# Optimization experiments

Measured on AMD Instinct MI355X. Metric: run time of the kernel, lower is better.

The kernel has to match this reference:

```python
import jax, jax.numpy as jnp
import numpy as np

D_MODEL = 128
VOCAB = 4096
N_LAYERS = 4
D_FF = 512
D_INNER = 2 * D_MODEL      # Mamba expand=2
D_STATE = 16               # Mamba default
D_CONV = 4                 # Mamba default
DT_RANK = 8                # ceil(d_model/16)
B, L = 8, 4096


def setup_inputs() -> dict:
    key = jax.random.key(0)
    ks = jax.random.split(key, 12)
    def n(k, shp, sc=0.02):
        return jax.random.normal(k, shp, dtype=jnp.float32) * sc
    A0 = jnp.tile(jnp.arange(1, D_STATE + 1, dtype=jnp.float32)[None, None, :], (N_LAYERS, D_INNER, 1))
    return {
        "tokens": jax.random.randint(ks[0], (B, L), 0, VOCAB),
        "emb": n(ks[1], (VOCAB, D_MODEL)),
        "ln_w": jnp.ones((N_LAYERS, D_MODEL), jnp.float32),
        "ln_b": jnp.zeros((N_LAYERS, D_MODEL), jnp.float32),
        "W_in": n(ks[2], (N_LAYERS, D_MODEL, 2 * D_INNER)),
        "conv_w": n(ks[3], (N_LAYERS, D_INNER, 1, D_CONV), 0.2),
        "conv_b": jnp.zeros((N_LAYERS, D_INNER), jnp.float32),
        "W_xproj": n(ks[4], (N_LAYERS, D_INNER, DT_RANK + 2 * D_STATE)),
        "W_dt": n(ks[5], (N_LAYERS, DT_RANK, D_INNER), 0.1),
        "b_dt": jnp.full((N_LAYERS, D_INNER), -4.6, jnp.float32),  # softplus ~ 0.01
        "A_log": jnp.log(A0),
        "D_skip": jnp.ones((N_LAYERS, D_INNER), jnp.float32),
        "W_out": n(ks[6], (N_LAYERS, D_INNER, D_MODEL)),
        "W1": n(ks[7], (D_MODEL, D_FF)),
        "b1": jnp.zeros((D_FF,), jnp.float32),
        "W2": n(ks[8], (D_FF, VOCAB)),
        "b2": jnp.zeros((VOCAB,), jnp.float32),
    }


def _layer_norm(x, w, b):
    mu = x.mean(-1, keepdims=True)
    var = ((x - mu) ** 2).mean(-1, keepdims=True)
    return (x - mu) * jax.lax.rsqrt(var + 1e-5) * w + b


def _mamba(x, W_in, conv_w, conv_b, W_xproj, W_dt, b_dt, A_log, D_skip, W_out):
    # x: [B, L, d_model]
    xz = jnp.einsum('bld,de->ble', x, W_in)          # [B, L, 2*d_inner]
    xc, z = jnp.split(xz, 2, axis=-1)
    # depthwise causal conv over time
    xt = xc.swapaxes(1, 2)                            # [B, d_inner, L]
    xt = jax.lax.conv_general_dilated(
        xt, conv_w, window_strides=(1,), padding=[(D_CONV - 1, 0)],
        feature_group_count=D_INNER,
        dimension_numbers=('NCH', 'OIH', 'NCH')) + conv_b[None, :, None]
    u = jax.nn.silu(xt).swapaxes(1, 2)                # [B, L, d_inner]
    dbc = jnp.einsum('bld,de->ble', u, W_xproj)
    dt_r = dbc[..., :DT_RANK]
    Bm = dbc[..., DT_RANK:DT_RANK + D_STATE]          # [B, L, d_state]
    Cm = dbc[..., DT_RANK + D_STATE:]                 # [B, L, d_state]
    dt = jax.nn.softplus(jnp.einsum('blr,rd->bld', dt_r, W_dt) + b_dt)
    A = -jnp.exp(A_log)                               # [d_inner, d_state]

    def step(h, t):
        dt_t, B_t, C_t, u_t = t                       # [B,di], [B,ds], [B,ds], [B,di]
        dA = jnp.exp(dt_t[..., None] * A)             # [B, di, ds]
        h = dA * h + (dt_t * u_t)[..., None] * B_t[:, None, :]
        y = jnp.einsum('bds,bs->bd', h, C_t)
        return h, y

    xs = (dt.swapaxes(0, 1), Bm.swapaxes(0, 1), Cm.swapaxes(0, 1), u.swapaxes(0, 1))
    h0 = jnp.zeros((x.shape[0], D_INNER, D_STATE), x.dtype)
    _, ys = jax.lax.scan(step, h0, xs)                # [L, B, d_inner]
    y = ys.swapaxes(0, 1) + u * D_skip
    y = y * jax.nn.silu(z)
    return jnp.einsum('bld,de->ble', y, W_out)


def reference(tokens, emb, ln_w, ln_b, W_in, conv_w, conv_b, W_xproj, W_dt,
              b_dt, A_log, D_skip, W_out, W1, b1, W2, b2):
    x = emb[tokens]                                   # [B, L, d_model]
    for i in range(N_LAYERS):
        # source discards the residual returned by Block: x = mixer(norm(x))
        x = _mamba(_layer_norm(x, ln_w[i], ln_b[i]), W_in[i], conv_w[i],
                   conv_b[i], W_xproj[i], W_dt[i], b_dt[i], A_log[i],
                   D_skip[i], W_out[i])
    h = jax.nn.relu(jnp.einsum('bld,df->blf', x, W1) + b1)
    return jnp.einsum('blf,fv->blv', h, W2) + b2
```

## Files before the change

### kernel.cpp

```cpp
#include <hip/hip_runtime.h>
#include <hip/hip_bf16.h>

typedef __hip_bfloat16 bf16;
typedef __attribute__((ext_vector_type(8))) short short8;
typedef __attribute__((ext_vector_type(4))) float floatx4;

#define D_MODEL 128
#define VOCAB   4096
#define N_LAYERS 4
#define D_FF    512
#define D_INNER 256
#define D_STATE 16
#define DT_RANK 8
#define BATCH   8
#define SEQ     4096
#define NTOK    (BATCH*SEQ)
#define NCHUNK  16
#define CHUNK   256

__device__ __forceinline__ float bf2f(bf16 v) { return __bfloat162float(v); }
__device__ __forceinline__ bf16  f2bf(float v) { return __float2bfloat16(v); }

__device__ __forceinline__ void load_lds16(const void* g, void* l) {
  __builtin_amdgcn_global_load_lds(
      (const __attribute__((address_space(1))) unsigned int*)g,
      (__attribute__((address_space(3))) unsigned int*)l, 16, 0, 0);
}

__device__ __forceinline__ void store_out(float* p, float v) { *p = v; }
__device__ __forceinline__ void store_out(bf16* p, float v) { *p = f2bf(v); }

#define WT_TOTAL 2686976
__global__ void convw_kernel(const float* __restrict__ W_in,
                             const float* __restrict__ W_xproj,
                             const float* __restrict__ W_out,
                             const float* __restrict__ W1,
                             const float* __restrict__ W2,
                             bf16* __restrict__ Wt) {
  for (int o = blockIdx.x * blockDim.x + threadIdx.x; o < WT_TOTAL;
       o += gridDim.x * blockDim.x) {
    float v;
    if (o < 262144) {
      int l = o >> 16, r = o & 65535, n = r >> 7, k = r & 127;
      v = W_in[l * 65536 + k * 512 + n];
    } else if (o < 393216) {
      int p = o - 262144, l = p >> 15, r = p & 32767, n = r >> 8, k = r & 255;
      v = (n < 40) ? W_xproj[l * 10240 + k * 40 + n] : 0.f;
    } else if (o < 524288) {
      int p = o - 393216, l = p >> 15, r = p & 32767, n = r >> 8, k = r & 255;
      v = W_out[l * 32768 + k * 128 + n];
    } else if (o < 589824) {
      int p = o - 524288, n = p >> 7, k = p & 127;
      v = W1[k * 512 + n];
    } else {
      int p = o - 589824, n = p >> 9, k = p & 511;
      v = W2[k * 4096 + n];
    }
    Wt[o] = f2bf(v);
  }
}

__global__ void embed_kernel(const int* __restrict__ tokens,
                             const float* __restrict__ emb,
                             float* __restrict__ X) {
  int idx = blockIdx.x * 256 + threadIdx.x;
  int bl = idx >> 5, c = idx & 31;
  int tok = tokens[bl];
  ((float4*)X)[(long)bl * 32 + c] = ((const float4*)emb)[(long)tok * 32 + c];
}

__global__ __launch_bounds__(256) void ln_kernel(const float* __restrict__ X,
                                                 const float* __restrict__ w,
                                                 const float* __restrict__ b,
                                                 bf16* __restrict__ XN) {
  int wv = threadIdx.x >> 6, lane = threadIdx.x & 63;
  long row = (long)blockIdx.x * 4 + wv;
  const float* xp = X + row * 128;
  float2 v = *(const float2*)(xp + lane * 2);
  float s = v.x + v.y, q = v.x * v.x + v.y * v.y;
  #pragma unroll
  for (int o = 32; o; o >>= 1) {
    s += __shfl_xor(s, o, 64);
    q += __shfl_xor(q, o, 64);
  }
  float mu = s * (1.f / 128.f);
  float var = q * (1.f / 128.f) - mu * mu;
  float rs = rsqrtf(var + 1e-5f);
  int c = lane * 2;
  float o0 = (v.x - mu) * rs * w[c] + b[c];
  float o1 = (v.y - mu) * rs * w[c + 1] + b[c + 1];
  bf16* op = XN + row * 128 + c;
  op[0] = f2bf(o0);
  op[1] = f2bf(o1);
}

template <typename OutT>
__global__ __launch_bounds__(256) void gemm_kernel(
    const bf16* __restrict__ A, const bf16* __restrict__ Bt,
    OutT* __restrict__ C, const float* __restrict__ bias,
    int K, int N, int relu) {
  __shared__ __align__(16) bf16 As[128 * 64];
  __shared__ __align__(16) bf16 Bs[128 * 64];
  const int tid = threadIdx.x;
  const int lane = tid & 63;
  const int wave = tid >> 6;
  const int m0 = blockIdx.x * 128;
  const int n0 = blockIdx.y * 128;
  const int wm = (wave >> 1) * 64;
  const int wn = (wave & 1) * 64;
  floatx4 acc[4][4] = {};

  const int lrow = lane >> 3;
  const int lcol = (lane & 7) * 8;
  for (int k0 = 0; k0 < K; k0 += 64) {
    #pragma unroll
    for (int j = 0; j < 4; ++j) {
      int qq = wave * 4 + j;
      int row = qq * 8 + lrow;
      load_lds16(A + (long)(m0 + row) * K + k0 + lcol, &As[(qq * 8) * 64]);
      load_lds16(Bt + (long)(n0 + row) * K + k0 + lcol, &Bs[(qq * 8) * 64]);
    }
    __syncthreads();
    #pragma unroll
    for (int kk = 0; kk < 64; kk += 32) {
      short8 af[4], bfr[4];
      const int fr = lane & 15;
      const int fq = (lane >> 4) * 8 + kk;
      #pragma unroll
      for (int i = 0; i < 4; ++i) {
        af[i]  = *(const short8*)&As[(wm + i * 16 + fr) * 64 + fq];
        bfr[i] = *(const short8*)&Bs[(wn + i * 16 + fr) * 64 + fq];
      }
      #pragma unroll
      for (int mi = 0; mi < 4; ++mi)
        #pragma unroll
        for (int ni = 0; ni < 4; ++ni)
          acc[mi][ni] = __builtin_amdgcn_mfma_f32_16x16x32_bf16(
              af[mi], bfr[ni], acc[mi][ni], 0, 0, 0);
    }
    __syncthreads();
  }
  const int cr = (lane >> 4) * 4;
  const int cc = lane & 15;
  #pragma unroll
  for (int ni = 0; ni < 4; ++ni) {
    int col = n0 + wn + ni * 16 + cc;
    if (col >= N) continue;
    float bv = bias ? bias[col] : 0.f;
    #pragma unroll
    for (int mi = 0; mi < 4; ++mi) {
      #pragma unroll
      for (int r = 0; r < 4; ++r) {
        int row = m0 + wm + mi * 16 + cr + r;
        float v = acc[mi][ni][r] + bv;
        if (relu) v = fmaxf(v, 0.f);
        store_out(&C[(long)row * N + col], v);
      }
    }
  }
}

__global__ __launch_bounds__(256) void conv_silu_kernel(
    const float* __restrict__ XZ, const float* __restrict__ conv_w,
    const float* __restrict__ conv_b, bf16* __restrict__ U,
    bf16* __restrict__ G) {
  int d = threadIdx.x;
  long bl = blockIdx.x;
  int t = (int)(bl & (SEQ - 1));
  float w0 = conv_w[d * 4 + 0], w1 = conv_w[d * 4 + 1];
  float w2 = conv_w[d * 4 + 2], w3 = conv_w[d * 4 + 3];
  const float* xp = XZ + bl * 512 + d;
  float acc = conv_b[d] + w3 * xp[0];
  if (t >= 1) acc += w2 * xp[-512];
  if (t >= 2) acc += w1 * xp[-1024];
  if (t >= 3) acc += w0 * xp[-1536];
  float su = acc / (1.f + __expf(-acc));
  float z = xp[256];
  float g = z / (1.f + __expf(-z));
  U[bl * 256 + d] = f2bf(su);
  G[bl * 256 + d] = f2bf(g);
}

__global__ __launch_bounds__(256) void dtprep_kernel(
    const float* __restrict__ DBC, const float* __restrict__ W_dt,
    const float* __restrict__ b_dt, float* __restrict__ DTo) {
  __shared__ float r8[8];
  int d = threadIdx.x;
  long bl = blockIdx.x;
  if (d < 8) r8[d] = DBC[bl * 40 + d];
  __syncthreads();
  float acc = b_dt[d];
  #pragma unroll
  for (int r = 0; r < 8; ++r) acc = fmaf(r8[r], W_dt[r * 256 + d], acc);
  float dt = (acc > 15.f) ? acc : log1pf(__expf(acc));
  DTo[bl * 256 + d] = dt;
}

__global__ __launch_bounds__(256) void scan_pass1_kernel(
    const float* __restrict__ DT, const bf16* __restrict__ U,
    const float* __restrict__ DBC, const float* __restrict__ A_log,
    float* __restrict__ CSP, float* __restrict__ CSS) {
  int s = threadIdx.x & 15, dd = threadIdx.x >> 4;
  int d = blockIdx.x * 16 + dd;
  int c = blockIdx.y, b = blockIdx.z;
  float A2 = -__expf(A_log[d * 16 + s]) * 1.44269504088896f;
  long t0 = (long)b * SEQ + (long)c * CHUNK;
  const float* dtp = DT + t0 * 256 + d;
  const bf16* up = U + t0 * 256 + d;
  const float* bp = DBC + t0 * 40 + 8 + s;
  float h = 0.f, P = 1.f;
  #pragma unroll 4
  for (int t = 0; t < CHUNK; ++t) {
    float dt = *dtp;
    float u = bf2f(*up);
    float Bv = *bp;
    float a = __builtin_amdgcn_exp2f(dt * A2);
    h = fmaf(a, h, dt * u * Bv);
    P *= a;
    dtp += 256; up += 256; bp += 40;
  }
  int idx = (b * 16 + c) * 4096 + d * 16 + s;
  CSP[idx] = P;
  CSS[idx] = h;
}

__global__ __launch_bounds__(256) void scan_combine_kernel(
    const float* __restrict__ P, const float* __restrict__ S,
    float* __restrict__ HI) {
  int id = blockIdx.x * 256 + threadIdx.x;
  int b = id >> 12, ds = id & 4095;
  float h = 0.f;
  #pragma unroll
  for (int c = 0; c < NCHUNK; ++c) {
    int idx = ((b * 16 + c) << 12) + ds;
    HI[idx] = h;
    h = S[idx] + P[idx] * h;
  }
}

__global__ __launch_bounds__(256) void scan_pass2_kernel(
    const float* __restrict__ DT, const bf16* __restrict__ U,
    const float* __restrict__ DBC, const bf16* __restrict__ G,
    const float* __restrict__ HI, const float* __restrict__ A_log,
    const float* __restrict__ D_skip, bf16* __restrict__ Y) {
  int s = threadIdx.x & 15, dd = threadIdx.x >> 4;
  int d = blockIdx.x * 16 + dd;
  int c = blockIdx.y, b = blockIdx.z;
  float A2 = -__expf(A_log[d * 16 + s]) * 1.44269504088896f;
  float Dv = D_skip[d];
  long t0 = (long)b * SEQ + (long)c * CHUNK;
  const float* dtp = DT + t0 * 256 + d;
  const bf16* up = U + t0 * 256 + d;
  const bf16* gp = G + t0 * 256 + d;
  const float* bp = DBC + t0 * 40 + 8 + s;
  bf16* yp = Y + t0 * 256 + d;
  int idx = (b * 16 + c) * 4096 + d * 16 + s;
  float h = HI[idx];
  #pragma unroll 4
  for (int t = 0; t < CHUNK; ++t) {
    float dt = *dtp;
    float u = bf2f(*up);
    float Bv = *bp;
    float Cv = bp[16];
    float a = __builtin_amdgcn_exp2f(dt * A2);
    h = fmaf(a, h, dt * u * Bv);
    float p = h * Cv;
    p += __shfl_xor(p, 8, 16);
    p += __shfl_xor(p, 4, 16);
    p += __shfl_xor(p, 2, 16);
    p += __shfl_xor(p, 1, 16);
    if (s == 0) {
      float g = bf2f(*gp);
      *yp = f2bf((p + u * Dv) * g);
    }
    dtp += 256; up += 256; gp += 256; bp += 40; yp += 256;
  }
}

extern "C" void kernel_launch(void* const* d_in, const int* in_sizes, int n_in,
                              void* d_out, int out_size, void* d_ws,
                              size_t ws_size, hipStream_t stream) {
  const int*   tokens  = (const int*)d_in[0];
  const float* emb     = (const float*)d_in[1];
  const float* ln_w    = (const float*)d_in[2];
  const float* ln_b    = (const float*)d_in[3];
  const float* W_in    = (const float*)d_in[4];
  const float* conv_w  = (const float*)d_in[5];
  const float* conv_b  = (const float*)d_in[6];
  const float* W_xproj = (const float*)d_in[7];
  const float* W_dt    = (const float*)d_in[8];
  const float* b_dt    = (const float*)d_in[9];
  const float* A_log   = (const float*)d_in[10];
  const float* D_skip  = (const float*)d_in[11];
  const float* W_out   = (const float*)d_in[12];
  const float* W1      = (const float*)d_in[13];
  const float* b1      = (const float*)d_in[14];
  const float* W2      = (const float*)d_in[15];
  const float* b2      = (const float*)d_in[16];

  char* ws = (char*)d_ws;
  float* X    = (float*)(ws + 0);
  float* XZ   = (float*)(ws + 16777216);
  bf16*  XN   = (bf16*) (ws + 83886080);
  bf16*  U    = (bf16*) (ws + 92274688);
  bf16*  G    = (bf16*) (ws + 109051904);
  float* DBC  = (float*)(ws + 125829120);
  float* DT   = (float*)(ws + 131072000);
  bf16*  Y    = (bf16*) (ws + 164626432);
  float* CSP  = (float*)(ws + 181403648);
  float* CSS  = (float*)(ws + 183500800);
  float* HI   = (float*)(ws + 185597952);
  bf16*  Wt   = (bf16*) (ws + 187695104);
  bf16*  H    = (bf16*) XZ;
  bf16*  XBF  = XN;

  bf16* Wt_in  = Wt;
  bf16* Wt_xp  = Wt + 262144;
  bf16* Wt_out = Wt + 393216;
  bf16* Wt_1   = Wt + 524288;
  bf16* Wt_2   = Wt + 589824;

  convw_kernel<<<2048, 256, 0, stream>>>(W_in, W_xproj, W_out, W1, W2, Wt);
  embed_kernel<<<4096, 256, 0, stream>>>(tokens, emb, X);

  for (int i = 0; i < N_LAYERS; ++i) {
    ln_kernel<<<8192, 256, 0, stream>>>(X, ln_w + i * 128, ln_b + i * 128, XN);
    gemm_kernel<float><<<dim3(256, 4), 256, 0, stream>>>(
        XN, Wt_in + i * 65536, XZ, nullptr, 128, 512, 0);
    conv_silu_kernel<<<32768, 256, 0, stream>>>(
        XZ, conv_w + i * 1024, conv_b + i * 256, U, G);
    gemm_kernel<float><<<dim3(256, 1), 256, 0, stream>>>(
        U, Wt_xp + i * 32768, DBC, nullptr, 256, 40, 0);
    dtprep_kernel<<<32768, 256, 0, stream>>>(
        DBC, W_dt + i * 2048, b_dt + i * 256, DT);
    scan_pass1_kernel<<<dim3(16, 16, 8), 256, 0, stream>>>(
        DT, U, DBC, A_log + i * 4096, CSP, CSS);
    scan_combine_kernel<<<128, 256, 0, stream>>>(CSP, CSS, HI);
    scan_pass2_kernel<<<dim3(16, 16, 8), 256, 0, stream>>>(
        DT, U, DBC, G, HI, A_log + i * 4096, D_skip + i * 256, Y);
    if (i < N_LAYERS - 1) {
      gemm_kernel<float><<<dim3(256, 1), 256, 0, stream>>>(
          Y, Wt_out + i * 32768, X, nullptr, 256, 128, 0);
    } else {
      gemm_kernel<bf16><<<dim3(256, 1), 256, 0, stream>>>(
          Y, Wt_out + i * 32768, XBF, nullptr, 256, 128, 0);
    }
  }

  gemm_kernel<bf16><<<dim3(256, 4), 256, 0, stream>>>(
      XBF, Wt_1, H, b1, 128, 512, 1);
  gemm_kernel<float><<<dim3(256, 32), 256, 0, stream>>>(
      H, Wt_2, (float*)d_out, b2, 512, 4096, 0);
}
```

Before: 2.325 ms.

## Add 256x256-tile double-buffered MFMA 32x32 GEMM for large projections

Adds a new GEMM kernel with 256x256 output tiles, 512 threads, and 32x32x16 bf16 MFMA instructions. It double-buffers LDS tiles via direct global-to-LDS loads with split-phase staging, uses an XOR swizzle for LDS reads, and remaps block indices to group tiles for cache locality. It replaces the in-projection, FFN first layer and the large vocab output GEMM, aiming for higher arithmetic intensity and better MFMA utilization. The cost is heavier register and LDS pressure, and the kernel assumes M and N divide evenly by 256.

```diff
diff --git a/kernel.cpp b/kernel.cpp
--- a/kernel.cpp
+++ b/kernel.cpp
@@ -4,6 +4,7 @@
 typedef __hip_bfloat16 bf16;
 typedef __attribute__((ext_vector_type(8))) short short8;
 typedef __attribute__((ext_vector_type(4))) float floatx4;
+typedef __attribute__((ext_vector_type(16))) float floatx16;
 
 #define D_MODEL 128
 #define VOCAB   4096
@@ -158,6 +159,129 @@
       }
     }
   }
+}
+
+template <typename OutT>
+__global__ __launch_bounds__(512, 2) void gemm256_kernel(
+    const bf16* __restrict__ A, const bf16* __restrict__ Bt,
+    OutT* __restrict__ C, const float* __restrict__ bias,
+    int K, int N, int ntiles, int relu) {
+  __shared__ __align__(16) bf16 sA[2][256 * 32];
+  __shared__ __align__(16) bf16 sB[2][256 * 32];
+  const int tid  = threadIdx.x;
+  const int lane = tid & 63;
+  const int wave = tid >> 6;
+  const int wm = (wave >> 2) << 7;
+  const int wn = (wave & 3) << 6;
+
+  const int nwg = gridDim.x;
+  const int cpx = nwg >> 3;
+  const int id  = ((int)blockIdx.x & 7) * cpx + ((int)blockIdx.x >> 3);
+  const int bm = id / ntiles, bn = id - bm * ntiles;
+  const long m0 = (long)bm << 8;
+  const long n0 = (long)bn << 8;
+
+  const bf16* Ab = A + m0 * K;
+  const bf16* Bb = Bt + n0 * K;
+
+  const int srow = lane >> 2;
+  const int sgl  = (((lane & 3) ^ (srow & 3)) << 3);
+  const int NT = K >> 5;
+
+  const int wh16  = (wave & 3) << 4;
+  const int aoff0 = (wave < 4) ? wh16 : (128 + wh16);
+  const int aoff1 = aoff0 + 64;
+
+#define STAGE(src, dst, r0, k0)                                           \
+  load_lds16((src) + (long)((r0) + srow) * K + (k0) + sgl, (dst) + (r0) * 32)
+
+  STAGE(Ab, sA[0], aoff0, 0);
+  STAGE(Bb, sB[0], aoff0, 0);
+  STAGE(Bb, sB[0], aoff1, 0);
+  STAGE(Ab, sA[0], aoff1, 0);
+
+  floatx16 acc[4][2] = {};
+  const int frow = lane & 31;
+  const int fg   = lane >> 5;
+
+  for (int t = 0; t < NT; ++t) {
+    const int cur = t & 1, nxt = cur ^ 1;
+    const int kn = (t + 1 < NT) ? ((t + 1) << 5) : 0;
+    const bf16* cA = sA[cur];
+    const bf16* cB = sB[cur];
+
+    asm volatile("s_waitcnt vmcnt(1)" ::: "memory");
+    asm volatile("s_barrier" ::: "memory");
+    STAGE(Ab, sA[nxt], aoff0, kn);
+    STAGE(Bb, sB[nxt], aoff0, kn);
+    short8 a0[2][2], b0[2][2];
+    #pragma unroll
+    for (int mi = 0; mi < 2; ++mi)
+      #pragma unroll
+      for (int kk = 0; kk < 2; ++kk) {
+        int r = wm + mi * 32 + frow;
+        int g = kk * 2 + fg;
+        a0[mi][kk] = *(const short8*)&cA[r * 32 + ((g ^ (r & 3)) << 3)];
+      }
+    #pragma unroll
+    for (int ni = 0; ni < 2; ++ni)
+      #pragma unroll
+      for (int kk = 0; kk < 2; ++kk) {
+        int r = wn + ni * 32 + frow;
+        int g = kk * 2 + fg;
+        b0[ni][kk] = *(const short8*)&cB[r * 32 + ((g ^ (r & 3)) << 3)];
+      }
+    __builtin_amdgcn_s_setprio(1);
+    #pragma unroll
+    for (int mi = 0; mi < 2; ++mi)
+      #pragma unroll
+      for (int ni = 0; ni < 2; ++ni)
+        #pragma unroll
+        for (int kk = 0; kk < 2; ++kk)
+          acc[mi][ni] = __builtin_amdgcn_mfma_f32_32x32x16_bf16(
+              a0[mi][kk], b0[ni][kk], acc[mi][ni], 0, 0, 0);
+    __builtin_amdgcn_s_setprio(0);
+
+    asm volatile("s_waitcnt vmcnt(2)" ::: "memory");
+    asm volatile("s_barrier" ::: "memory");
+    STAGE(Bb, sB[nxt], aoff1, kn);
+    STAGE(Ab, sA[nxt], aoff1, kn);
+    short8 a1[2][2];
+    #pragma unroll
+    for (int mi = 0; mi < 2; ++mi)
+      #pragma unroll
+      for (int kk = 0; kk < 2; ++kk) {
+        int r = wm + 64 + mi * 32 + frow;
+        int g = kk * 2 + fg;
+        a1[mi][kk] = *(const short8*)&cA[r * 32 + ((g ^ (r & 3)) << 3)];
+      }
+    __builtin_amdgcn_s_setprio(1);
+    #pragma unroll
+    for (int mi = 0; mi < 2; ++mi)
+      #pragma unroll
+      for (int ni = 0; ni < 2; ++ni)
+        #pragma unroll
+        for (int kk = 0; kk < 2; ++kk)
+          acc[2 + mi][ni] = __builtin_amdgcn_mfma_f32_32x32x16_bf16(
+              a1[mi][kk], b0[ni][kk], acc[2 + mi][ni], 0, 0, 0);
+    __builtin_amdgcn_s_setprio(0);
+  }
+#undef STAGE
+
+  #pragma unroll
+  for (int mi = 0; mi < 4; ++mi)
+    #pragma unroll
+    for (int ni = 0; ni < 2; ++ni) {
+      long col = n0 + wn + ni * 32 + frow;
+      float bv = bias ? bias[col] : 0.f;
+      #pragma unroll
+      for (int r = 0; r < 16; ++r) {
+        long row = m0 + wm + mi * 32 + (r & 3) + ((r >> 2) << 3) + (fg << 2);
+        float v = acc[mi][ni][r] + bv;
+        if (relu) v = fmaxf(v, 0.f);
+        store_out(&C[row * N + col], v);
+      }
+    }
 }
 
 __global__ __launch_bounds__(256) void conv_silu_kernel(
@@ -325,8 +449,8 @@
 
   for (int i = 0; i < N_LAYERS; ++i) {
     ln_kernel<<<8192, 256, 0, stream>>>(X, ln_w + i * 128, ln_b + i * 128, XN);
-    gemm_kernel<float><<<dim3(256, 4), 256, 0, stream>>>(
-        XN, Wt_in + i * 65536, XZ, nullptr, 128, 512, 0);
+    gemm256_kernel<float><<<256, 512, 0, stream>>>(
+        XN, Wt_in + i * 65536, XZ, nullptr, 128, 512, 2, 0);
     conv_silu_kernel<<<32768, 256, 0, stream>>>(
         XZ, conv_w + i * 1024, conv_b + i * 256, U, G);
     gemm_kernel<float><<<dim3(256, 1), 256, 0, stream>>>(
@@ -347,8 +471,8 @@
     }
   }
 
-  gemm_kernel<bf16><<<dim3(256, 4), 256, 0, stream>>>(
-      XBF, Wt_1, H, b1, 128, 512, 1);
-  gemm_kernel<float><<<dim3(256, 32), 256, 0, stream>>>(
-      H, Wt_2, (float*)d_out, b2, 512, 4096, 0);
-}
+  gemm256_kernel<bf16><<<256, 512, 0, stream>>>(
+      XBF, Wt_1, H, b1, 128, 512, 2, 1);
+  gemm256_kernel<float><<<2048, 512, 0, stream>>>(
+      H, Wt_2, (float*)d_out, b2, 512, 4096, 16, 0);
+}
```

Result: faster. 2.213 ms (-4.9%).
